# Kernel optimization log

Measured on AMD Instinct MI355X. Metric: run time of the kernel, lower is better.

## Reference

```python
import jax, jax.numpy as jnp
import numpy as np

DIM = 1024
HEADS = 16
HEAD_DIM = DIM // HEADS
MLP = 4 * DIM
EPS = 1e-5


def layer_norm(x, g, b):
    mu = jnp.mean(x, axis=-1, keepdims=True)
    var = jnp.var(x, axis=-1, keepdims=True)
    return (x - mu) * jax.lax.rsqrt(var + EPS) * g + b


def rope_cos_sin(n, d):
    inv_freq = 1.0 / (10000.0 ** (jnp.arange(0, d, 2, dtype=jnp.float32) / d))
    t = jnp.arange(n, dtype=jnp.float32)
    freqs = jnp.outer(t, inv_freq)          # [N, d/2]
    emb = jnp.concatenate([freqs, freqs], -1)  # [N, d]
    return jnp.cos(emb), jnp.sin(emb)


def rotate_half(x):
    x1, x2 = x[..., ::2], x[..., 1::2]
    return jnp.concatenate([-x2, x1], axis=-1)


def setup_inputs() -> dict:
    key = jax.random.key(0)
    ks = jax.random.split(key, 16)
    B, N = 2, 2048
    s = lambda fan_in: 1.0 / np.sqrt(fan_in)
    inp = {
        "x": jax.random.normal(ks[0], (B, N, DIM), jnp.float32),
        "t_emb": jax.random.normal(ks[1], (B, DIM), jnp.float32),
        "norm1_g": jnp.ones((DIM,), jnp.float32),
        "norm1_b": jnp.zeros((DIM,), jnp.float32),
        "Wq": jax.random.normal(ks[2], (DIM, DIM), jnp.float32) * s(DIM),
        "Wk": jax.random.normal(ks[3], (DIM, DIM), jnp.float32) * s(DIM),
        "Wv": jax.random.normal(ks[4], (DIM, DIM), jnp.float32) * s(DIM),
        "Wo": jax.random.normal(ks[5], (DIM, DIM), jnp.float32) * s(DIM),
        "norm2_g": jnp.ones((DIM,), jnp.float32),
        "norm2_b": jnp.zeros((DIM,), jnp.float32),
        "W1": jax.random.normal(ks[6], (DIM, MLP), jnp.float32) * s(DIM),
        "W2": jax.random.normal(ks[7], (MLP, DIM), jnp.float32) * s(MLP),
        "ada_W": jax.random.normal(ks[8], (DIM, 6 * DIM), jnp.float32) * s(DIM),
        "ada_b": jnp.zeros((6 * DIM,), jnp.float32),
    }
    return inp


def reference(x, t_emb, norm1_g, norm1_b, Wq, Wk, Wv, Wo,
              norm2_g, norm2_b, W1, W2, ada_W, ada_b):
    B, N, C = x.shape
    H, D = HEADS, HEAD_DIM
    scale = D ** -0.5

    mod = jax.nn.silu(t_emb) @ ada_W + ada_b          # [B, 6C]
    (shift_msa, scale_msa, gate_msa,
     shift_mlp, scale_mlp, gate_mlp) = jnp.split(mod, 6, axis=-1)

    xn = layer_norm(x, norm1_g, norm1_b) * (1 + scale_msa[:, None, :]) + shift_msa[:, None, :]

    q = (xn @ Wq).reshape(B, N, H, D).transpose(0, 2, 1, 3)  # [B,H,N,D]
    k = (xn @ Wk).reshape(B, N, H, D).transpose(0, 2, 1, 3)
    v = (xn @ Wv).reshape(B, N, H, D).transpose(0, 2, 1, 3)

    cos, sin = rope_cos_sin(N, D)                     # [N, D]
    q = q * cos + rotate_half(q) * sin
    k = k * cos + rotate_half(k) * sin

    attn = jnp.einsum('bhnd,bhmd->bhnm', q, k) * scale  # explicit O(N^2) scores
    attn = jax.nn.softmax(attn, axis=-1)
    out = jnp.einsum('bhnm,bhmd->bhnd', attn, v)

    out = out.transpose(0, 2, 1, 3).reshape(B, N, C) @ Wo
    x = x + gate_msa[:, None, :] * out

    xn = layer_norm(x, norm2_g, norm2_b) * (1 + scale_mlp[:, None, :]) + shift_mlp[:, None, :]
    mlp = jax.nn.gelu(xn @ W1, approximate=False) @ W2
    x = x + gate_mlp[:, None, :] * mlp
    return x
```

## Files before the change

### kernel.cpp

```cpp
#include <hip/hip_runtime.h>
#include <math.h>

#define BB    2
#define NN    2048
#define CDIM  1024
#define HEADS 16
#define HDIM  64
#define MLPD  4096
#define MODC  6144
#define EPSV  1e-5f
#define LOG2E 1.4426950408889634f
#define MSPLIT 16

typedef __attribute__((ext_vector_type(8))) short s8v;
typedef __attribute__((ext_vector_type(4))) float f4v;

__device__ inline unsigned short f2bf(float f) {
  union { float f; unsigned u; } v; v.f = f;
  unsigned r = v.u + 0x7FFFu + ((v.u >> 16) & 1u);
  return (unsigned short)(r >> 16);
}
__device__ inline float bf2f(unsigned short h) {
  union { unsigned u; float f; } v; v.u = ((unsigned)h) << 16;
  return v.f;
}

__global__ __launch_bounds__(256) void mod_part(
    const float* __restrict__ t_emb, const float* __restrict__ ada_W,
    float* __restrict__ part) {
  int j = blockIdx.x * 256 + threadIdx.x;
  int b = blockIdx.y, ks = blockIdx.z;
  __shared__ float st[64];
  if (threadIdx.x < 64) {
    float v = t_emb[b * CDIM + ks * 64 + threadIdx.x];
    st[threadIdx.x] = v / (1.0f + expf(-v));
  }
  __syncthreads();
  float acc = 0.f;
  const float* wp = ada_W + (size_t)(ks * 64) * MODC + j;
  #pragma unroll 8
  for (int i = 0; i < 64; ++i) acc += st[i] * wp[(size_t)i * MODC];
  part[((size_t)ks * BB + b) * MODC + j] = acc;
}

__global__ __launch_bounds__(256) void mod_reduce(
    const float* __restrict__ part, const float* __restrict__ ada_b,
    float* __restrict__ mod) {
  int idx = blockIdx.x * 256 + threadIdx.x;
  int b = idx / MODC, j = idx % MODC;
  float a = ada_b[j];
  #pragma unroll
  for (int s = 0; s < MSPLIT; ++s) a += part[((size_t)s * BB + b) * MODC + j];
  mod[(size_t)b * MODC + j] = a;
}

__device__ inline float wave_sum64(float v) {
  for (int o = 32; o > 0; o >>= 1) v += __shfl_down(v, o, 64);
  return v;
}

__global__ __launch_bounds__(256) void ln_mod_bf16(
    const float* __restrict__ x, const float* __restrict__ g,
    const float* __restrict__ bta, const float* __restrict__ mod,
    int shift_off, int scale_off, unsigned short* __restrict__ out) {
  int r = blockIdx.x;
  int b = r / NN;
  int t = threadIdx.x;
  const float* xr = x + (size_t)r * CDIM;
  float4 xv = ((const float4*)xr)[t];
  float s  = xv.x + xv.y + xv.z + xv.w;
  float s2 = xv.x*xv.x + xv.y*xv.y + xv.z*xv.z + xv.w*xv.w;
  __shared__ float ws1[4], ws2[4];
  float sw = wave_sum64(s), s2w = wave_sum64(s2);
  int lane = t & 63, wid = t >> 6;
  if (lane == 0) { ws1[wid] = sw; ws2[wid] = s2w; }
  __syncthreads();
  float mu  = (ws1[0] + ws1[1] + ws1[2] + ws1[3]) * (1.0f / CDIM);
  float var = (ws2[0] + ws2[1] + ws2[2] + ws2[3]) * (1.0f / CDIM) - mu * mu;
  float rstd = rsqrtf(var + EPSV);
  const float* mods = mod + (size_t)b * MODC;
  float4 gv = ((const float4*)g)[t];
  float4 bv = ((const float4*)bta)[t];
  float4 sc = ((const float4*)(mods + scale_off))[t];
  float4 sh = ((const float4*)(mods + shift_off))[t];
  ushort4 ov;
  ov.x = f2bf(((xv.x - mu) * rstd * gv.x + bv.x) * (1.0f + sc.x) + sh.x);
  ov.y = f2bf(((xv.y - mu) * rstd * gv.y + bv.y) * (1.0f + sc.y) + sh.y);
  ov.z = f2bf(((xv.z - mu) * rstd * gv.z + bv.z) * (1.0f + sc.z) + sh.z);
  ov.w = f2bf(((xv.w - mu) * rstd * gv.w + bv.w) * (1.0f + sc.w) + sh.w);
  ((ushort4*)(out + (size_t)r * CDIM))[t] = ov;
}

__global__ __launch_bounds__(256) void wcast_all(
    const float* __restrict__ Wq, const float* __restrict__ Wk,
    const float* __restrict__ Wv, const float* __restrict__ Wo,
    const float* __restrict__ W1, const float* __restrict__ W2,
    unsigned short* __restrict__ Wqkvt, unsigned short* __restrict__ Wot,
    unsigned short* __restrict__ W1t, unsigned short* __restrict__ W2t) {
  int bid = blockIdx.x;
  const float* W; unsigned short* Wt; int K, N, t;
  if (bid < 4096) {
    int m = bid >> 10;
    t = bid & 1023;
    K = CDIM; N = CDIM;
    W  = (m == 0) ? Wq : (m == 1) ? Wk : (m == 2) ? Wv : Wo;
    Wt = (m == 3) ? Wot : (Wqkvt + (size_t)m * CDIM * CDIM);
  } else if (bid < 8192) {
    t = bid - 4096; K = CDIM; N = MLPD; W = W1; Wt = W1t;
  } else {
    t = bid - 8192; K = MLPD; N = CDIM; W = W2; Wt = W2t;
  }
  int ntiles = N >> 5;
  int n0 = (t % ntiles) * 32, k0 = (t / ntiles) * 32;
  __shared__ float tile[32][33];
  int tx = threadIdx.x & 31, ty = threadIdx.x >> 5;
  #pragma unroll
  for (int p = 0; p < 4; ++p)
    tile[ty + p * 8][tx] = W[(size_t)(k0 + ty + p * 8) * N + n0 + tx];
  __syncthreads();
  #pragma unroll
  for (int p = 0; p < 4; ++p)
    Wt[(size_t)(n0 + ty + p * 8) * K + k0 + tx] = f2bf(tile[tx][ty + p * 8]);
}

__global__ __launch_bounds__(256) void mfma_gemm(
    const unsigned short* __restrict__ A,
    const unsigned short* __restrict__ Bt,
    int M, int N, int K,
    unsigned short* __restrict__ Ob, unsigned short* __restrict__ Ob2,
    unsigned short* __restrict__ Ob3, int mode) {
  __shared__ unsigned short As[128 * 32];
  __shared__ unsigned short Bs[128 * 32];
  int tid = threadIdx.x;
  int wave = tid >> 6, lane = tid & 63;
  int quad = lane >> 4, l15 = lane & 15;
  int m0 = blockIdx.y * 128, n0 = blockIdx.x * 128;
  int wm = (wave >> 1) * 64, wn = (wave & 1) * 64;

  f4v acc[4][4] = {};
  int srow = lane >> 2;
  int scol = (lane & 3) * 8;

  for (int k0 = 0; k0 < K; k0 += 32) {
    __syncthreads();
    #pragma unroll
    for (int s = 0; s < 2; ++s) {
      int inst = 2 * wave + s;
      const unsigned short* ga =
          A + (size_t)(m0 + inst * 16 + srow) * K + k0 + scol;
      __builtin_amdgcn_global_load_lds(
          (const __attribute__((address_space(1))) unsigned int*)(const void*)ga,
          (__attribute__((address_space(3))) unsigned int*)(void*)(As + inst * 512),
          16, 0, 0);
      const unsigned short* gb =
          Bt + (size_t)(n0 + inst * 16 + srow) * K + k0 + scol;
      __builtin_amdgcn_global_load_lds(
          (const __attribute__((address_space(1))) unsigned int*)(const void*)gb,
          (__attribute__((address_space(3))) unsigned int*)(void*)(Bs + inst * 512),
          16, 0, 0);
    }
    __syncthreads();

    s8v af[4], bf[4];
    #pragma unroll
    for (int i = 0; i < 4; ++i)
      af[i] = *(const s8v*)(As + ((wm + i * 16 + l15) * 32 + quad * 8));
    #pragma unroll
    for (int j = 0; j < 4; ++j)
      bf[j] = *(const s8v*)(Bs + ((wn + j * 16 + l15) * 32 + quad * 8));
    #pragma unroll
    for (int i = 0; i < 4; ++i)
      #pragma unroll
      for (int j = 0; j < 4; ++j)
        acc[i][j] = __builtin_amdgcn_mfma_f32_16x16x32_bf16(
            af[i], bf[j], acc[i][j], 0, 0, 0);
  }

  #pragma unroll
  for (int i = 0; i < 4; ++i) {
    int rbase = m0 + wm + i * 16 + quad * 4;
    #pragma unroll
    for (int j = 0; j < 4; ++j) {
      int c = n0 + wn + j * 16 + l15;
      #pragma unroll
      for (int rg = 0; rg < 4; ++rg) {
        int r = rbase + rg;
        float v = acc[i][j][rg];
        if (mode == 0) {
          unsigned short* dst = (c < 1024) ? Ob : ((c < 2048) ? Ob2 : Ob3);
          dst[(size_t)r * 1024 + (c & 1023)] = f2bf(v);
        } else {
          v = 0.5f * v * (1.0f + erff(v * 0.70710678118f));
          Ob[(size_t)r * N + c] = f2bf(v);
        }
      }
    }
  }
}

__global__ __launch_bounds__(1024) void mfma_gemm_res(
    const unsigned short* __restrict__ A,
    const unsigned short* __restrict__ Bt,
    int M, int N, int K,
    float* __restrict__ O0,
    const float* __restrict__ res, const float* __restrict__ mod,
    int gate_off) {
  __shared__ unsigned short SH[3 * 16384];
  int tid = threadIdx.x;
  int wave = tid >> 6, lane = tid & 63;
  int quad = lane >> 4, l15 = lane & 15;
  int m0 = blockIdx.y * 128, n0 = blockIdx.x * 128;
  int pos = wave & 7;
  int om = pos >> 1, on = pos & 1;
  int ks = wave >> 3;

  f4v acc[2][4] = {};

  int srow = lane >> 3;
  int ksrc = ((lane & 7) ^ (lane >> 3)) << 3;
  const int nt = K >> 6;

  #define STAGE_RES(T, BUF)                                                    \
    {                                                                          \
      int k0_ = (T) << 6;                                                      \
      unsigned short* dsta = SH + (BUF) * 16384 + wave * 512;                  \
      const unsigned short* ga =                                               \
          A + (size_t)(m0 + 8 * wave + srow) * K + k0_ + ksrc;                 \
      __builtin_amdgcn_global_load_lds(                                        \
          (const __attribute__((address_space(1))) unsigned int*)(const void*)ga, \
          (__attribute__((address_space(3))) unsigned int*)(void*)dsta,        \
          16, 0, 0);                                                           \
      const unsigned short* gb =                                               \
          Bt + (size_t)(n0 + 8 * wave + srow) * K + k0_ + ksrc;                \
      __builtin_amdgcn_global_load_lds(                                        \
          (const __attribute__((address_space(1))) unsigned int*)(const void*)gb, \
          (__attribute__((address_space(3))) unsigned int*)(void*)(dsta + 8192), \
          16, 0, 0);                                                           \
    }

  STAGE_RES(0, 0);
  STAGE_RES(1, 1);
  asm volatile("s_waitcnt vmcnt(2)" ::: "memory");
  __syncthreads();

  int kx = (ks * 32 + quad * 8) ^ ((l15 & 7) << 3);

  int rbuf = 0, sbuf = 2;
  for (int t = 0; t < nt; ++t) {
    if (t + 2 < nt) STAGE_RES(t + 2, sbuf);

    const unsigned short* base = SH + rbuf * 16384;
    s8v af[2], bf[4];
    #pragma unroll
    for (int i = 0; i < 2; ++i)
      af[i] = *(const s8v*)(base + (om * 32 + i * 16 + l15) * 64 + kx);
    #pragma unroll
    for (int j = 0; j < 4; ++j)
      bf[j] = *(const s8v*)(base + 8192 + (on * 64 + j * 16 + l15) * 64 + kx);
    #pragma unroll
    for (int i = 0; i < 2; ++i)
      #pragma unroll
      for (int j = 0; j < 4; ++j)
        acc[i][j] = __builtin_amdgcn_mfma_f32_16x16x32_bf16(
            af[i], bf[j], acc[i][j], 0, 0, 0);

    if (t + 2 < nt) {
      asm volatile("s_waitcnt vmcnt(2)" ::: "memory");
    } else if (t + 1 < nt) {
      asm volatile("s_waitcnt vmcnt(0)" ::: "memory");
    }
    __syncthreads();
    rbuf = (rbuf == 2) ? 0 : rbuf + 1;
    sbuf = (sbuf == 2) ? 0 : sbuf + 1;
  }
  #undef STAGE_RES

  float* red = (float*)SH;
  if (wave >= 8) {
    int rb = (wave - 8) * 2304 + lane * 36;
    #pragma unroll
    for (int i = 0; i < 2; ++i)
      #pragma unroll
      for (int j = 0; j < 4; ++j)
        *(f4v*)(red + rb + (i * 4 + j) * 4) = acc[i][j];
  }
  __syncthreads();
  if (wave < 8) {
    int rb = wave * 2304 + lane * 36;
    #pragma unroll
    for (int i = 0; i < 2; ++i)
      #pragma unroll
      for (int j = 0; j < 4; ++j)
        acc[i][j] += *(const f4v*)(red + rb + (i * 4 + j) * 4);
    #pragma unroll
    for (int i = 0; i < 2; ++i) {
      int rbase = m0 + om * 32 + i * 16 + quad * 4;
      #pragma unroll
      for (int j = 0; j < 4; ++j) {
        int c = n0 + on * 64 + j * 16 + l15;
        #pragma unroll
        for (int rg = 0; rg < 4; ++rg) {
          int r = rbase + rg;
          int bb2 = r >> 11;
          O0[(size_t)r * N + c] =
              res[(size_t)r * N + c] + mod[bb2 * MODC + gate_off + c] * acc[i][j][rg];
        }
      }
    }
  }
}

__global__ __launch_bounds__(256) void rope_qk(
    unsigned short* __restrict__ qb, const unsigned short* __restrict__ kb,
    unsigned short* __restrict__ kpack, float qscale) {
  int r = blockIdx.x;
  int b = r / NN, n = r % NN;
  int t = threadIdx.x;
  int isK = blockIdx.y;
  const unsigned short* src = isK ? kb : qb;
  float scale = isK ? 1.0f : qscale;
  __shared__ float row[CDIM];
  __shared__ float csv[32], snv[32];
  if (t < 32) {
    float invf = powf(10000.0f, -(float)t / 32.0f);
    float sn, cs;
    sincosf((float)n * invf, &sn, &cs);
    csv[t] = cs * scale; snv[t] = sn * scale;
  }
  const unsigned short* qr = src + (size_t)r * CDIM;
  ushort4 xv = ((const ushort4*)qr)[t];
  row[t * 4 + 0] = bf2f(xv.x);
  row[t * 4 + 1] = bf2f(xv.y);
  row[t * 4 + 2] = bf2f(xv.z);
  row[t * 4 + 3] = bf2f(xv.w);
  __syncthreads();
  unsigned short o[4];
  int c0 = t * 4;
  #pragma unroll
  for (int q4 = 0; q4 < 4; ++q4) {
    int c = c0 + q4;
    int h = c >> 6, d = c & 63;
    int i = d & 31;
    float rh = (d < 32) ? -row[h * 64 + 2 * d + 1] : row[h * 64 + 2 * (d - 32)];
    o[q4] = f2bf(row[c] * csv[i] + rh * snv[i]);
  }
  if (!isK) {
    ((ushort4*)(qb + (size_t)r * CDIM))[t] = make_ushort4(o[0], o[1], o[2], o[3]);
  } else {
    int h = c0 >> 6, d0 = c0 & 63;
    int half = d0 >> 5, quad = (d0 >> 3) & 3, j0 = d0 & 7;
    int bh = b * HEADS + h;
    int tt = n >> 6, kt = (n >> 4) & 3, l15 = n & 15;
    int lane = quad * 16 + l15;
    size_t off = ((((size_t)bh * 32 + tt) * 8 + kt * 2 + half) * 64 + lane) * 8 + j0;
    unsigned int lo = (unsigned)o[0] | ((unsigned)o[1] << 16);
    unsigned int hi = (unsigned)o[2] | ((unsigned)o[3] << 16);
    *(uint2*)(kpack + off) = make_uint2(lo, hi);
  }
}

__global__ __launch_bounds__(256) void vtrans_pack(
    const unsigned short* __restrict__ vrow, unsigned short* __restrict__ vpack) {
  int t = blockIdx.x;
  int bh = blockIdx.y;
  int b = bh >> 4, h = bh & 15;
  __shared__ unsigned short L[64 * 72];
  int tid = threadIdx.x;
  #pragma unroll
  for (int p = 0; p < 2; ++p) {
    int c = tid + p * 256;
    int key = c >> 3, dc = (c & 7) * 8;
    *(s8v*)(L + key * 72 + dc) =
        *(const s8v*)(vrow + (size_t)(b * NN + t * 64 + key) * CDIM + h * HDIM + dc);
  }
  __syncthreads();
  #pragma unroll
  for (int p = 0; p < 2; ++p) {
    int o = tid + p * 256;
    int f = o >> 6, lane = o & 63;
    int dt = f >> 1, half = f & 1, quad = lane >> 4, l15 = lane & 15;
    int d = dt * 16 + l15;
    unsigned short tmp[8];
    #pragma unroll
    for (int j = 0; j < 8; ++j) {
      int key = (j & 3) * 16 + half * 8 + quad * 2 + (j >> 2);
      tmp[j] = L[key * 72 + d];
    }
    *(s8v*)(vpack + ((((size_t)bh * 32 + t) * 8 + f) * 64 + lane) * 8) = *(s8v*)tmp;
  }
}

__global__ __launch_bounds__(512, 4) void fattn_pack(
    const unsigned short* __restrict__ qb,
    const unsigned short* __restrict__ kpack,
    const unsigned short* __restrict__ vpack,
    unsigned short* __restrict__ ob) {
  int bid = blockIdx.x;
  int qt = bid >> 5, bh = bid & 31;
  int b = bh >> 4, h = bh & 15;
  int tid = threadIdx.x;
  int wave = tid >> 6, lane = tid & 63;
  int quad = lane >> 4, l15 = lane & 15;

  __shared__ unsigned short smem[16384 + 8 * 1152];
  unsigned short* Pw = smem + 16384 + wave * 1152;

  int n0 = qt * 128;
  int qrow = n0 + wave * 16 + l15;
  s8v qf[2];
  {
    const unsigned short* qp = qb + (size_t)(b * NN + qrow) * CDIM + h * HDIM;
    qf[0] = *(const s8v*)(qp + quad * 8);
    qf[1] = *(const s8v*)(qp + 32 + quad * 8);
  }

  f4v acc[4] = {};
  float m_i[4], l_i[4];
  #pragma unroll
  for (int r = 0; r < 4; ++r) { m_i[r] = -1e30f; l_i[r] = 0.f; }

  const unsigned short* ksrc = kpack + (size_t)bh * 131072 + wave * 512 + lane * 8;
  const unsigned short* vsrc = vpack + (size_t)bh * 131072 + wave * 512 + lane * 8;

  #define STAGE_ATT(T, BUF)                                                    \
    {                                                                          \
      __builtin_amdgcn_global_load_lds(                                        \
          (const __attribute__((address_space(1))) unsigned int*)(const void*)(ksrc + (size_t)(T) * 4096), \
          (__attribute__((address_space(3))) unsigned int*)(void*)(smem + (BUF) * 8192 + wave * 512), \
          16, 0, 0);                                                           \
      __builtin_amdgcn_global_load_lds(                                        \
          (const __attribute__((address_space(1))) unsigned int*)(const void*)(vsrc + (size_t)(T) * 4096), \
          (__attribute__((address_space(3))) unsigned int*)(void*)(smem + (BUF) * 8192 + 4096 + wave * 512), \
          16, 0, 0);                                                           \
    }

  STAGE_ATT(0, 0);
  asm volatile("s_waitcnt vmcnt(0)" ::: "memory");
  __syncthreads();

  int buf = 0;
  for (int t = 0; t < NN / 64; ++t) {
    if (t + 1 < NN / 64) STAGE_ATT(t + 1, buf ^ 1);

    const unsigned short* kb_ = smem + buf * 8192 + lane * 8;
    const unsigned short* vb_ = kb_ + 4096;
    s8v kf[8], vf[8];
    #pragma unroll
    for (int f = 0; f < 8; ++f) kf[f] = *(const s8v*)(kb_ + f * 512);
    #pragma unroll
    for (int f = 0; f < 8; ++f) vf[f] = *(const s8v*)(vb_ + f * 512);

    f4v s4[4] = {};
    #pragma unroll
    for (int kt = 0; kt < 4; ++kt) {
      s4[kt] = __builtin_amdgcn_mfma_f32_16x16x32_bf16(qf[0], kf[kt * 2], s4[kt], 0, 0, 0);
      s4[kt] = __builtin_amdgcn_mfma_f32_16x16x32_bf16(qf[1], kf[kt * 2 + 1], s4[kt], 0, 0, 0);
    }

    #pragma unroll
    for (int r = 0; r < 4; ++r) {
      float mv = fmaxf(fmaxf(s4[0][r], s4[1][r]), fmaxf(s4[2][r], s4[3][r]));
      #pragma unroll
      for (int msk = 1; msk < 16; msk <<= 1)
        mv = fmaxf(mv, __shfl_xor(mv, msk, 64));
      float mnew = fmaxf(m_i[r], mv);
      float alpha = __builtin_amdgcn_exp2f(m_i[r] - mnew);
      m_i[r] = mnew;
      float ls = 0.f;
      #pragma unroll
      for (int kt = 0; kt < 4; ++kt) {
        float p = __builtin_amdgcn_exp2f(s4[kt][r] - mnew);
        s4[kt][r] = p;
        ls += p;
      }
      l_i[r] = l_i[r] * alpha + ls;
      acc[0][r] *= alpha; acc[1][r] *= alpha;
      acc[2][r] *= alpha; acc[3][r] *= alpha;
    }

    #pragma unroll
    for (int r = 0; r < 4; ++r) {
      unsigned int lo = (__float_as_uint(s4[0][r]) >> 16) |
                        (__float_as_uint(s4[1][r]) & 0xffff0000u);
      unsigned int hi = (__float_as_uint(s4[2][r]) >> 16) |
                        (__float_as_uint(s4[3][r]) & 0xffff0000u);
      *(uint2*)(Pw + (quad * 4 + r) * 72 + l15 * 4) = make_uint2(lo, hi);
    }

    s8v pf0 = *(const s8v*)(Pw + l15 * 72 + quad * 8);
    s8v pf1 = *(const s8v*)(Pw + l15 * 72 + 32 + quad * 8);

    #pragma unroll
    for (int dt = 0; dt < 4; ++dt) {
      acc[dt] = __builtin_amdgcn_mfma_f32_16x16x32_bf16(pf0, vf[dt * 2], acc[dt], 0, 0, 0);
      acc[dt] = __builtin_amdgcn_mfma_f32_16x16x32_bf16(pf1, vf[dt * 2 + 1], acc[dt], 0, 0, 0);
    }

    if (t + 1 < NN / 64) {
      asm volatile("s_waitcnt vmcnt(0)" ::: "memory");
      __syncthreads();
      buf ^= 1;
    }
  }
  #undef STAGE_ATT

  #pragma unroll
  for (int r = 0; r < 4; ++r) {
    float l = l_i[r];
    #pragma unroll
    for (int msk = 1; msk < 16; msk <<= 1)
      l += __shfl_xor(l, msk, 64);
    float inv = 1.0f / l;
    size_t row = (size_t)(b * NN + n0 + wave * 16 + quad * 4 + r);
    unsigned short* op = ob + row * CDIM + h * HDIM;
    #pragma unroll
    for (int dt = 0; dt < 4; ++dt)
      op[dt * 16 + l15] = f2bf(acc[dt][r] * inv);
  }
}

extern "C" void kernel_launch(void* const* d_in, const int* in_sizes, int n_in,
                              void* d_out, int out_size, void* d_ws, size_t ws_size,
                              hipStream_t stream) {
  const float* x    = (const float*)d_in[0];
  const float* temb = (const float*)d_in[1];
  const float* n1g  = (const float*)d_in[2];
  const float* n1b  = (const float*)d_in[3];
  const float* Wq   = (const float*)d_in[4];
  const float* Wk   = (const float*)d_in[5];
  const float* Wv   = (const float*)d_in[6];
  const float* Wo   = (const float*)d_in[7];
  const float* n2g  = (const float*)d_in[8];
  const float* n2b  = (const float*)d_in[9];
  const float* W1   = (const float*)d_in[10];
  const float* W2   = (const float*)d_in[11];
  const float* adaW = (const float*)d_in[12];
  const float* adab = (const float*)d_in[13];
  float* out = (float*)d_out;

  const size_t TOK = (size_t)BB * NN * CDIM;
  float* wsf = (float*)d_ws;
  float* mod     = wsf;
  float* modpart = wsf + 16384;
  unsigned short* tokb  = (unsigned short*)(wsf + 16384 + MSPLIT * BB * MODC);
  unsigned short* qb    = tokb + TOK;
  unsigned short* kb    = qb + TOK;
  unsigned short* kpack = kb + TOK;
  unsigned short* vpack = kpack + TOK;
  unsigned short* Wqkvt = vpack + TOK;
  unsigned short* Wot   = Wqkvt + 3 * CDIM * CDIM;
  unsigned short* W1t   = Wot + CDIM * CDIM;
  unsigned short* W2t   = W1t + CDIM * MLPD;
  unsigned short* h1b   = W2t + MLPD * CDIM;
  unsigned short* vrow  = h1b;
  float* x1 = (float*)qb;

  const int M = BB * NN;

  mod_part<<<dim3(MODC / 256, BB, MSPLIT), 256, 0, stream>>>(temb, adaW, modpart);
  mod_reduce<<<dim3(BB * MODC / 256), 256, 0, stream>>>(modpart, adab, mod);
  ln_mod_bf16<<<dim3(M), 256, 0, stream>>>(x, n1g, n1b, mod, 0, 1024, tokb);

  wcast_all<<<dim3(12288), 256, 0, stream>>>(
      Wq, Wk, Wv, Wo, W1, W2, Wqkvt, Wot, W1t, W2t);

  mfma_gemm<<<dim3(24, 32), 256, 0, stream>>>(
      tokb, Wqkvt, M, 3 * CDIM, CDIM, qb, kb, vrow, 0);

  rope_qk<<<dim3(M, 2), 256, 0, stream>>>(qb, kb, kpack, 0.125f * LOG2E);

  vtrans_pack<<<dim3(NN / 64, BB * HEADS), 256, 0, stream>>>(vrow, vpack);

  fattn_pack<<<dim3((NN / 128) * BB * HEADS), 512, 0, stream>>>(
      qb, kpack, vpack, tokb);

  mfma_gemm_res<<<dim3(CDIM / 128, M / 128), 1024, 0, stream>>>(
      tokb, Wot, M, CDIM, CDIM, x1, x, mod, 2048);

  ln_mod_bf16<<<dim3(M), 256, 0, stream>>>(x1, n2g, n2b, mod, 3072, 4096, tokb);

  mfma_gemm<<<dim3(MLPD / 128, M / 128), 256, 0, stream>>>(
      tokb, W1t, M, MLPD, CDIM, h1b, nullptr, nullptr, 1);

  mfma_gemm_res<<<dim3(CDIM / 128, M / 128), 1024, 0, stream>>>(
      h1b, W2t, M, CDIM, MLPD, out, x1, mod, 5120);
}
```

Measured before the change: 427.6 us.

## Rewrite QKV and MLP-up GEMMs with 1024-thread triple-buffered split-K pipeline

Replaces the 256-thread single-buffered bf16 MFMA GEMM used for the QKV projection and the first MLP matmul with a 1024-thread variant. It stages 64-wide K tiles into a triple-buffered LDS ring with XOR-swizzled layout, issuing loads two tiles ahead. Sixteen waves split the K dimension in two halves and reduce through shared memory before the epilogue. This aims to hide global-load latency and cut LDS bank conflicts and per-iteration barriers, at the cost of more LDS (96KB), lower occupancy per CU, and an extra reduction step.

```diff
diff --git a/kernel.cpp b/kernel.cpp
--- a/kernel.cpp
+++ b/kernel.cpp
@@ -123,75 +123,116 @@
     Wt[(size_t)(n0 + ty + p * 8) * K + k0 + tx] = f2bf(tile[tx][ty + p * 8]);
 }
 
-__global__ __launch_bounds__(256) void mfma_gemm(
+__global__ __launch_bounds__(1024) void mfma_gemm_big(
     const unsigned short* __restrict__ A,
     const unsigned short* __restrict__ Bt,
     int M, int N, int K,
     unsigned short* __restrict__ Ob, unsigned short* __restrict__ Ob2,
     unsigned short* __restrict__ Ob3, int mode) {
-  __shared__ unsigned short As[128 * 32];
-  __shared__ unsigned short Bs[128 * 32];
+  __shared__ unsigned short SH[3 * 16384];
   int tid = threadIdx.x;
   int wave = tid >> 6, lane = tid & 63;
   int quad = lane >> 4, l15 = lane & 15;
   int m0 = blockIdx.y * 128, n0 = blockIdx.x * 128;
-  int wm = (wave >> 1) * 64, wn = (wave & 1) * 64;
-
-  f4v acc[4][4] = {};
-  int srow = lane >> 2;
-  int scol = (lane & 3) * 8;
-
-  for (int k0 = 0; k0 < K; k0 += 32) {
-    __syncthreads();
-    #pragma unroll
-    for (int s = 0; s < 2; ++s) {
-      int inst = 2 * wave + s;
-      const unsigned short* ga =
-          A + (size_t)(m0 + inst * 16 + srow) * K + k0 + scol;
-      __builtin_amdgcn_global_load_lds(
-          (const __attribute__((address_space(1))) unsigned int*)(const void*)ga,
-          (__attribute__((address_space(3))) unsigned int*)(void*)(As + inst * 512),
-          16, 0, 0);
-      const unsigned short* gb =
-          Bt + (size_t)(n0 + inst * 16 + srow) * K + k0 + scol;
-      __builtin_amdgcn_global_load_lds(
-          (const __attribute__((address_space(1))) unsigned int*)(const void*)gb,
-          (__attribute__((address_space(3))) unsigned int*)(void*)(Bs + inst * 512),
-          16, 0, 0);
-    }
-    __syncthreads();
-
-    s8v af[4], bf[4];
-    #pragma unroll
-    for (int i = 0; i < 4; ++i)
-      af[i] = *(const s8v*)(As + ((wm + i * 16 + l15) * 32 + quad * 8));
+  int pos = wave & 7;
+  int om = pos >> 1, on = pos & 1;
+  int ks = wave >> 3;
+
+  f4v acc[2][4] = {};
+
+  int srow = lane >> 3;
+  int ksrc = ((lane & 7) ^ (lane >> 3)) << 3;
+  const int nt = K >> 6;
+
+  #define STAGE_BIG(T, BUF)                                                    \
+    {                                                                          \
+      int k0_ = (T) << 6;                                                      \
+      unsigned short* dsta = SH + (BUF) * 16384 + wave * 512;                  \
+      const unsigned short* ga =                                               \
+          A + (size_t)(m0 + 8 * wave + srow) * K + k0_ + ksrc;                 \
+      __builtin_amdgcn_global_load_lds(                                        \
+          (const __attribute__((address_space(1))) unsigned int*)(const void*)ga, \
+          (__attribute__((address_space(3))) unsigned int*)(void*)dsta,        \
+          16, 0, 0);                                                           \
+      const unsigned short* gb =                                               \
+          Bt + (size_t)(n0 + 8 * wave + srow) * K + k0_ + ksrc;                \
+      __builtin_amdgcn_global_load_lds(                                        \
+          (const __attribute__((address_space(1))) unsigned int*)(const void*)gb, \
+          (__attribute__((address_space(3))) unsigned int*)(void*)(dsta + 8192), \
+          16, 0, 0);                                                           \
+    }
+
+  STAGE_BIG(0, 0);
+  STAGE_BIG(1, 1);
+  asm volatile("s_waitcnt vmcnt(2)" ::: "memory");
+  __syncthreads();
+
+  int kx = (ks * 32 + quad * 8) ^ ((l15 & 7) << 3);
+
+  int rbuf = 0, sbuf = 2;
+  for (int t = 0; t < nt; ++t) {
+    if (t + 2 < nt) STAGE_BIG(t + 2, sbuf);
+
+    const unsigned short* base = SH + rbuf * 16384;
+    s8v af[2], bf[4];
+    #pragma unroll
+    for (int i = 0; i < 2; ++i)
+      af[i] = *(const s8v*)(base + (om * 32 + i * 16 + l15) * 64 + kx);
     #pragma unroll
     for (int j = 0; j < 4; ++j)
-      bf[j] = *(const s8v*)(Bs + ((wn + j * 16 + l15) * 32 + quad * 8));
-    #pragma unroll
-    for (int i = 0; i < 4; ++i)
+      bf[j] = *(const s8v*)(base + 8192 + (on * 64 + j * 16 + l15) * 64 + kx);
+    #pragma unroll
+    for (int i = 0; i < 2; ++i)
       #pragma unroll
       for (int j = 0; j < 4; ++j)
         acc[i][j] = __builtin_amdgcn_mfma_f32_16x16x32_bf16(
             af[i], bf[j], acc[i][j], 0, 0, 0);
-  }
-
-  #pragma unroll
-  for (int i = 0; i < 4; ++i) {
-    int rbase = m0 + wm + i * 16 + quad * 4;
-    #pragma unroll
-    for (int j = 0; j < 4; ++j) {
-      int c = n0 + wn + j * 16 + l15;
-      #pragma unroll
-      for (int rg = 0; rg < 4; ++rg) {
-        int r = rbase + rg;
-        float v = acc[i][j][rg];
-        if (mode == 0) {
-          unsigned short* dst = (c < 1024) ? Ob : ((c < 2048) ? Ob2 : Ob3);
-          dst[(size_t)r * 1024 + (c & 1023)] = f2bf(v);
-        } else {
-          v = 0.5f * v * (1.0f + erff(v * 0.70710678118f));
-          Ob[(size_t)r * N + c] = f2bf(v);
+
+    if (t + 2 < nt) {
+      asm volatile("s_waitcnt vmcnt(2)" ::: "memory");
+    } else if (t + 1 < nt) {
+      asm volatile("s_waitcnt vmcnt(0)" ::: "memory");
+    }
+    __syncthreads();
+    rbuf = (rbuf == 2) ? 0 : rbuf + 1;
+    sbuf = (sbuf == 2) ? 0 : sbuf + 1;
+  }
+  #undef STAGE_BIG
+
+  float* red = (float*)SH;
+  if (wave >= 8) {
+    int rb = (wave - 8) * 2304 + lane * 36;
+    #pragma unroll
+    for (int i = 0; i < 2; ++i)
+      #pragma unroll
+      for (int j = 0; j < 4; ++j)
+        *(f4v*)(red + rb + (i * 4 + j) * 4) = acc[i][j];
+  }
+  __syncthreads();
+  if (wave < 8) {
+    int rb = wave * 2304 + lane * 36;
+    #pragma unroll
+    for (int i = 0; i < 2; ++i)
+      #pragma unroll
+      for (int j = 0; j < 4; ++j)
+        acc[i][j] += *(const f4v*)(red + rb + (i * 4 + j) * 4);
+    #pragma unroll
+    for (int i = 0; i < 2; ++i) {
+      int rbase = m0 + om * 32 + i * 16 + quad * 4;
+      #pragma unroll
+      for (int j = 0; j < 4; ++j) {
+        int c = n0 + on * 64 + j * 16 + l15;
+        #pragma unroll
+        for (int rg = 0; rg < 4; ++rg) {
+          int r = rbase + rg;
+          float v = acc[i][j][rg];
+          if (mode == 0) {
+            unsigned short* dst = (c < 1024) ? Ob : ((c < 2048) ? Ob2 : Ob3);
+            dst[(size_t)r * 1024 + (c & 1023)] = f2bf(v);
+          } else {
+            v = 0.5f * v * (1.0f + erff(v * 0.70710678118f));
+            Ob[(size_t)r * N + c] = f2bf(v);
+          }
         }
       }
     }
@@ -564,7 +605,7 @@
   wcast_all<<<dim3(12288), 256, 0, stream>>>(
       Wq, Wk, Wv, Wo, W1, W2, Wqkvt, Wot, W1t, W2t);
 
-  mfma_gemm<<<dim3(24, 32), 256, 0, stream>>>(
+  mfma_gemm_big<<<dim3(24, 32), 1024, 0, stream>>>(
       tokb, Wqkvt, M, 3 * CDIM, CDIM, qb, kb, vrow, 0);
 
   rope_qk<<<dim3(M, 2), 256, 0, stream>>>(qb, kb, kpack, 0.125f * LOG2E);
@@ -579,7 +620,7 @@
 
   ln_mod_bf16<<<dim3(M), 256, 0, stream>>>(x1, n2g, n2b, mod, 3072, 4096, tokb);
 
-  mfma_gemm<<<dim3(MLPD / 128, M / 128), 256, 0, stream>>>(
+  mfma_gemm_big<<<dim3(MLPD / 128, M / 128), 1024, 0, stream>>>(
       tokb, W1t, M, MLPD, CDIM, h1b, nullptr, nullptr, 1);
 
   mfma_gemm_res<<<dim3(CDIM / 128, M / 128), 1024, 0, stream>>>(
```

After: 428.7 us. About the same (+0.3%).
